# Kernel optimization log

Hardware: AMD Instinct MI355X
Metric: run time of the kernel (lower is better)

Reference implementation:

```python
import jax, jax.numpy as jnp
import numpy as np

B, T, D1, D2, DM, V, K = 2, 512, 256, 128, 1024, 32000, 4
SCALE = 0.05  # keep tanh/sigmoid out of full saturation with randn params


def setup_inputs() -> dict:
    key = jax.random.key(0)
    ks = jax.random.split(key, 7)
    s = lambda k, shape: SCALE * jax.random.normal(k, shape, dtype=jnp.float32)
    return {
        "gc": jax.random.normal(ks[0], (B, T, D1), dtype=jnp.float32),
        "H": s(ks[1], (K, DM, D1)),
        "U": s(ks[2], (K, D2, D1)),
        "v": s(ks[3], (V, D2)),
        "u": s(ks[4], (K, D1)),
        "b": s(ks[5], (V, K)),
        "emb": s(ks[6], (V, DM)),
    }


def reference(gc, H, U, v, u, b, emb):
    # gc: (B,T,D1)
    hc = jnp.tanh(jnp.einsum('kdi,bti->btkd', H, gc))        # (B,T,K,DM)
    tU = jnp.tanh(jnp.einsum('kji,bti->btkj', U, gc))        # (B,T,K,D2)
    # token- and context-dependent gate logits: (B,T,V,K)
    lc = (jnp.einsum('vj,btkj->btvk', v, tU)
          + jnp.einsum('ki,bti->btk', u, gc)[:, :, None, :]
          + b[None, None])
    gamma = jax.nn.sigmoid(lc[..., :K - 1])                  # (B,T,V,3)
    g0, g1, g2 = gamma[..., 0], gamma[..., 1], gamma[..., 2]
    # sigmoid-tree mixture priors: (B,T,V,K)
    pi = jnp.stack([g0 * g1, g0 * (1.0 - g1),
                    (1.0 - g0) * g2, (1.0 - g0) * (1.0 - g2)], axis=-1)
    # contract hc with embeddings per gate FIRST (avoids btikj blow-up),
    # then weight by pi -- same math as the original pi (x) emb outer product.
    dots = jnp.einsum('btkd,vd->btvk', hc, emb)              # (B,T,V,K)
    logits = jnp.sum(pi * dots, axis=-1)                     # (B,T,V)
    return jax.nn.softmax(logits, axis=-1)
```

## Files before the change

kernel.cpp:

```cpp
#include <hip/hip_runtime.h>
#include <math.h>

namespace {

typedef _Float16 f16;
typedef _Float16 f16x8 __attribute__((ext_vector_type(8)));
typedef float    f32x4 __attribute__((ext_vector_type(4)));

constexpr int kBT = 1024, kD1 = 256, kD2 = 128, kDM = 1024, kV = 32000, kK = 4;
constexpr int AR = kBT * kK;
constexpr int ROWS_H = kK * kDM;
constexpr int ROWS_U = kK * kD2;
constexpr int ROWS_ALL = ROWS_H + ROWS_U + kK;
constexpr int SLICES = 8;
constexpr int SLICE_ROWS = (ROWS_ALL + SLICES - 1) / SLICES;
constexpr int NBY = kV / 128;

__global__ __launch_bounds__(256) void prep_gemm(
    const float* __restrict__ gc, const float* __restrict__ Hm,
    const float* __restrict__ Um, const float* __restrict__ um,
    f16* __restrict__ hc, f16* __restrict__ tu, float* __restrict__ ug)
{
    __shared__ float sgc[8][kD1];
    const int btBase = blockIdx.x * 8;
    for (int idx = threadIdx.x; idx < 8 * kD1; idx += 256)
        sgc[idx / kD1][idx % kD1] = gc[(size_t)btBase * kD1 + idx];
    __syncthreads();

    const int rStart = blockIdx.y * SLICE_ROWS;
    int rEnd = rStart + SLICE_ROWS;
    if (rEnd > ROWS_ALL) rEnd = ROWS_ALL;
    for (int r = rStart + (int)threadIdx.x; r < rEnd; r += 256) {
        const float* wrow;
        if (r < ROWS_H)               wrow = Hm + (size_t)r * kD1;
        else if (r < ROWS_H + ROWS_U) wrow = Um + (size_t)(r - ROWS_H) * kD1;
        else                          wrow = um + (size_t)(r - ROWS_H - ROWS_U) * kD1;

        float acc[8] = {0.f,0.f,0.f,0.f,0.f,0.f,0.f,0.f};
        for (int i = 0; i < kD1; i += 4) {
            const float4 w = *reinterpret_cast<const float4*>(wrow + i);
            #pragma unroll
            for (int b = 0; b < 8; ++b) {
                const float4 g = *reinterpret_cast<const float4*>(&sgc[b][i]);
                acc[b] = fmaf(w.x, g.x, acc[b]);
                acc[b] = fmaf(w.y, g.y, acc[b]);
                acc[b] = fmaf(w.z, g.z, acc[b]);
                acc[b] = fmaf(w.w, g.w, acc[b]);
            }
        }
        #pragma unroll
        for (int b = 0; b < 8; ++b) {
            const int bt = btBase + b;
            if (r < ROWS_H) {
                const int k = r >> 10, d = r & 1023;
                hc[((size_t)(bt * kK + k) << 10) + d] = (f16)tanhf(acc[b]);
            } else if (r < ROWS_H + ROWS_U) {
                const int r2 = r - ROWS_H;
                const int k = r2 >> 7, j = r2 & 127;
                tu[(size_t)(bt * kK + k) * kD2 + j] = (f16)tanhf(acc[b]);
            } else {
                ug[bt * kK + (r - ROWS_H - ROWS_U)] = acc[b];
            }
        }
    }
}

__global__ __launch_bounds__(256) void cvt_kernel(
    const float* __restrict__ src, f16* __restrict__ dst, int n8)
{
    const int i = blockIdx.x * 256 + threadIdx.x;
    if (i >= n8) return;
    const float4 x0 = *reinterpret_cast<const float4*>(src + (size_t)i * 8);
    const float4 x1 = *reinterpret_cast<const float4*>(src + (size_t)i * 8 + 4);
    union { f16 h[8]; uint4 v; } u;
    u.h[0] = (f16)x0.x; u.h[1] = (f16)x0.y; u.h[2] = (f16)x0.z; u.h[3] = (f16)x0.w;
    u.h[4] = (f16)x1.x; u.h[5] = (f16)x1.y; u.h[6] = (f16)x1.z; u.h[7] = (f16)x1.w;
    *reinterpret_cast<uint4*>(dst + (size_t)i * 8) = u.v;
}

__device__ __forceinline__ uint packf16x2(float a, float b) {
    union { f16 h[2]; uint u; } z;
    z.h[0] = (f16)a; z.h[1] = (f16)b;
    return z.u;
}

__global__ __launch_bounds__(256, 2) void fused_mfma(
    const f16* __restrict__ hc,  const f16* __restrict__ tu,
    const f16* __restrict__ v16, const f16* __restrict__ e16,
    const float* __restrict__ ug, const float* __restrict__ bmat,
    f16* __restrict__ lg16, float* __restrict__ psum)
{
    __shared__ __align__(16) f16 sA[2][128 * 64];
    __shared__ __align__(16) f16 sB[2][128 * 64];

    const int tid  = threadIdx.x;
    const int lane = tid & 63;
    const int wave = tid >> 6;
    const int fr = lane & 15, fq = lane >> 4;
    const int wrow = wave >> 1, wcol = wave & 1;
    const int aRowBase = blockIdx.x * 128;
    const int vBase    = blockIdx.y * 128;
    const int btB      = blockIdx.x * 32 + wrow * 16;

    const int srow = lane >> 3;
    const int scol = ((lane & 7) ^ srow) * 8;

    const f16* gApt = tu  + (size_t)(aRowBase + wave * 32 + srow) * kD2 + scol;
    const f16* gBpt = v16 + (size_t)(vBase    + wave * 32 + srow) * kD2 + scol;
    const f16* sApt = hc  + (size_t)(aRowBase + wave * 32 + srow) * kDM + scol;
    const f16* sBpt = e16 + (size_t)(vBase    + wave * 32 + srow) * kDM + scol;

    f16* dA = &sA[0][0] + wave * 4 * 512;
    f16* dB = &sB[0][0] + wave * 4 * 512;

#define GLD(SRC, DST)                                                         \
    __builtin_amdgcn_global_load_lds(                                         \
        (const __attribute__((address_space(1))) void*)(SRC),                 \
        (__attribute__((address_space(3))) void*)(DST), 16, 0, 0)

    auto stage_gate = [&](int t) {
        #pragma unroll
        for (int i = 0; i < 4; ++i) {
            GLD(gApt + t * 64 + i * 8 * kD2, dA + t * 8192 + i * 512);
            GLD(gBpt + t * 64 + i * 8 * kD2, dB + t * 8192 + i * 512);
        }
    };
    auto stage_dots = [&](int buf) {
        #pragma unroll
        for (int i = 0; i < 4; ++i) {
            GLD(sApt + i * 8 * kDM, dA + buf * 8192 + i * 512);
            GLD(sBpt + i * 8 * kDM, dB + buf * 8192 + i * 512);
        }
        sApt += 64; sBpt += 64;
    };

    const int ps0 = (fq ^ (fr & 7)) * 8;
    const int ps1 = ((4 + fq) ^ (fr & 7)) * 8;
    const f16* rA0 = &sA[0][0] + (wrow * 64 + fr) * 64 + ps0;
    const f16* rA1 = &sA[0][0] + (wrow * 64 + fr) * 64 + ps1;
    const f16* rB0 = &sB[0][0] + (wcol * 64 + fr) * 64 + ps0;
    const f16* rB1 = &sB[0][0] + (wcol * 64 + fr) * 64 + ps1;

    auto mmStep = [&](f32x4 (&acc)[4][4], int q) {
        const int qo = q * 8192;
        {
            f16x8 a[4], b[4];
            #pragma unroll
            for (int m = 0; m < 4; ++m)
                a[m] = *reinterpret_cast<const f16x8*>(rA0 + qo + m * 1024);
            #pragma unroll
            for (int n = 0; n < 4; ++n)
                b[n] = *reinterpret_cast<const f16x8*>(rB0 + qo + n * 1024);
            __builtin_amdgcn_s_setprio(1);
            #pragma unroll
            for (int m = 0; m < 4; ++m)
                #pragma unroll
                for (int n = 0; n < 4; ++n)
                    acc[m][n] = __builtin_amdgcn_mfma_f32_16x16x32_f16(
                        a[m], b[n], acc[m][n], 0, 0, 0);
            __builtin_amdgcn_s_setprio(0);
        }
        {
            f16x8 a[4], b[4];
            #pragma unroll
            for (int m = 0; m < 4; ++m)
                a[m] = *reinterpret_cast<const f16x8*>(rA1 + qo + m * 1024);
            #pragma unroll
            for (int n = 0; n < 4; ++n)
                b[n] = *reinterpret_cast<const f16x8*>(rB1 + qo + n * 1024);
            __builtin_amdgcn_s_setprio(1);
            #pragma unroll
            for (int m = 0; m < 4; ++m)
                #pragma unroll
                for (int n = 0; n < 4; ++n)
                    acc[m][n] = __builtin_amdgcn_mfma_f32_16x16x32_f16(
                        a[m], b[n], acc[m][n], 0, 0, 0);
            __builtin_amdgcn_s_setprio(0);
        }
    };

#define WAITBAR(VM)                                                           \
    asm volatile("s_waitcnt vmcnt(" VM ")" ::: "memory");                     \
    __builtin_amdgcn_s_barrier();                                             \
    asm volatile("" ::: "memory");
#define ENDBAR                                                                \
    asm volatile("" ::: "memory");                                            \
    __builtin_amdgcn_s_barrier();                                             \
    asm volatile("" ::: "memory");

    const f32x4 zz = {0.f, 0.f, 0.f, 0.f};

    f32x4 gacc[4][4];
    #pragma unroll
    for (int m = 0; m < 4; ++m)
        #pragma unroll
        for (int n = 0; n < 4; ++n) gacc[m][n] = zz;

    stage_gate(0);
    stage_gate(1);          WAITBAR("8")  mmStep(gacc, 0);  ENDBAR
    stage_dots(0);          WAITBAR("8")  mmStep(gacc, 1);  ENDBAR

    uint pi01[4][4], pi23[4][4];
    {
        float4 bb[4];
        #pragma unroll
        for (int n = 0; n < 4; ++n)
            bb[n] = *reinterpret_cast<const float4*>(
                bmat + (size_t)(vBase + wcol * 64 + n * 16 + fr) * 4);
        #pragma unroll
        for (int m = 0; m < 4; ++m) {
            const float4 ugv = *reinterpret_cast<const float4*>(
                ug + (btB + m * 4 + fq) * 4);
            #pragma unroll
            for (int n = 0; n < 4; ++n) {
                const float l0 = gacc[m][n][0] + ugv.x + bb[n].x;
                const float l1 = gacc[m][n][1] + ugv.y + bb[n].y;
                const float l2 = gacc[m][n][2] + ugv.z + bb[n].z;
                const float g0 = 1.f / (1.f + __expf(-l0));
                const float g1 = 1.f / (1.f + __expf(-l1));
                const float g2 = 1.f / (1.f + __expf(-l2));
                pi01[m][n] = packf16x2(g0 * g1, g0 * (1.f - g1));
                pi23[m][n] = packf16x2((1.f - g0) * g2, (1.f - g0) * (1.f - g2));
            }
        }
    }

    f32x4 dacc[4][4];
    #pragma unroll
    for (int m = 0; m < 4; ++m)
        #pragma unroll
        for (int n = 0; n < 4; ++n) dacc[m][n] = zz;

    for (int it = 0; it < 7; ++it) {
        stage_dots(1);      WAITBAR("8")  mmStep(dacc, 0);  ENDBAR
        stage_dots(0);      WAITBAR("8")  mmStep(dacc, 1);  ENDBAR
    }
    stage_dots(1);          WAITBAR("8")  mmStep(dacc, 0);  ENDBAR
                            WAITBAR("0")  mmStep(dacc, 1);
#undef WAITBAR
#undef ENDBAR
#undef GLD

    #pragma unroll
    for (int m = 0; m < 4; ++m) {
        const int bt = btB + m * 4 + fq;
        float es = 0.f;
        #pragma unroll
        for (int n = 0; n < 4; ++n) {
            const int v = vBase + wcol * 64 + n * 16 + fr;
            union { uint u; f16 h[2]; } p01, p23;
            p01.u = pi01[m][n]; p23.u = pi23[m][n];
            const float lg = (float)p01.h[0] * dacc[m][n][0]
                           + (float)p01.h[1] * dacc[m][n][1]
                           + (float)p23.h[0] * dacc[m][n][2]
                           + (float)p23.h[1] * dacc[m][n][3];
            const f16 lh = (f16)lg;
            lg16[(size_t)bt * kV + v] = lh;
            es += __expf((float)lh);
        }
        es += __shfl_xor(es, 1);
        es += __shfl_xor(es, 2);
        es += __shfl_xor(es, 4);
        es += __shfl_xor(es, 8);
        if (fr == 0)
            psum[(size_t)bt * 512 + blockIdx.y * 2 + wcol] = es;
    }
}

__global__ __launch_bounds__(256) void softmax_kernel(
    float* __restrict__ out, const f16* __restrict__ lg16,
    const float* __restrict__ psum)
{
    __shared__ float red[4];
    const int bt = blockIdx.x;
    const f16* row16 = lg16 + (size_t)bt * kV;
    float* row = out + (size_t)bt * kV;
    const int tid = threadIdx.x;

    float s = 0.f;
    for (int i = tid; i < 2 * NBY; i += 256) s += psum[(size_t)bt * 512 + i];
    #pragma unroll
    for (int o = 1; o < 64; o <<= 1) s += __shfl_xor(s, o);
    if ((tid & 63) == 0) red[tid >> 6] = s;
    __syncthreads();
    s = red[0] + red[1] + red[2] + red[3];
    const float inv = 1.f / s;

    for (int i = tid * 8; i < kV; i += 2048) {
        union { uint4 v; f16 h[8]; } u;
        u.v = *reinterpret_cast<const uint4*>(row16 + i);
        float4 y0, y1;
        y0.x = __expf((float)u.h[0]) * inv;
        y0.y = __expf((float)u.h[1]) * inv;
        y0.z = __expf((float)u.h[2]) * inv;
        y0.w = __expf((float)u.h[3]) * inv;
        y1.x = __expf((float)u.h[4]) * inv;
        y1.y = __expf((float)u.h[5]) * inv;
        y1.z = __expf((float)u.h[6]) * inv;
        y1.w = __expf((float)u.h[7]) * inv;
        *reinterpret_cast<float4*>(row + i)     = y0;
        *reinterpret_cast<float4*>(row + i + 4) = y1;
    }
}

}

extern "C" void kernel_launch(void* const* d_in, const int* in_sizes, int n_in,
                              void* d_out, int out_size, void* d_ws, size_t ws_size,
                              hipStream_t stream)
{
    (void)in_sizes; (void)n_in; (void)out_size; (void)ws_size;
    const float* gc   = (const float*)d_in[0];
    const float* Hm   = (const float*)d_in[1];
    const float* Um   = (const float*)d_in[2];
    const float* vmat = (const float*)d_in[3];
    const float* um   = (const float*)d_in[4];
    const float* bmat = (const float*)d_in[5];
    const float* emb  = (const float*)d_in[6];
    float* out = (float*)d_out;

    size_t off = 0;
    auto take = [&](size_t bytes) -> char* {
        char* p = (char*)d_ws + off;
        off += (bytes + 255) & ~(size_t)255;
        return p;
    };
    f16*   hc   = (f16*)  take((size_t)AR * kDM * 2);
    f16*   tu   = (f16*)  take((size_t)AR * kD2 * 2);
    f16*   v16  = (f16*)  take((size_t)kV * kD2 * 2);
    f16*   e16  = (f16*)  take((size_t)kV * kDM * 2);
    float* ug   = (float*)take((size_t)AR * 4);
    float* psum = (float*)take((size_t)kBT * 512 * 4);
    f16*   lg16 = (f16*)  take((size_t)kBT * kV * 2);

    prep_gemm<<<dim3(kBT / 8, SLICES), 256, 0, stream>>>(gc, Hm, Um, um, hc, tu, ug);
    cvt_kernel<<<(kV * kD2 / 8 + 255) / 256, 256, 0, stream>>>(vmat, v16, kV * kD2 / 8);
    cvt_kernel<<<(kV * kDM / 8 + 255) / 256, 256, 0, stream>>>(emb, e16, kV * kDM / 8);
    fused_mfma<<<dim3(AR / 128, NBY), 256, 0, stream>>>(
        hc, tu, v16, e16, ug, bmat, lg16, psum);
    softmax_kernel<<<dim3(kBT), 256, 0, stream>>>(out, lg16, psum);
}
```

Before: 533.7 us.

## Halve MFMA K-tile to 32 and merge prep and convert kernels

The main GEMM kernel's LDS K-tile shrinks from 64 to 32 halves per stage. That halves shared memory per block and drops the 2-blocks-per-SM launch bound, aiming for higher occupancy. The swizzle, load mapping and pipeline (twice as many stages, with a different vmcnt wait) are reworked to match. The three preprocessing launches (projection GEMM plus two fp32-to-fp16 conversions) are merged into one kernel to save launch overhead and let them run concurrently. The cost is more barriers per unit of work and less MFMA work between each synchronisation.

```diff
diff --git a/kernel.cpp b/kernel.cpp
--- a/kernel.cpp
+++ b/kernel.cpp
@@ -16,18 +16,48 @@
 constexpr int SLICE_ROWS = (ROWS_ALL + SLICES - 1) / SLICES;
 constexpr int NBY = kV / 128;
 
-__global__ __launch_bounds__(256) void prep_gemm(
+constexpr int PREP_BLOCKS = (kBT / 8) * SLICES;
+constexpr int CVTV_BLOCKS = (kV * kD2 / 8) / 256;
+constexpr int CVTE_BLOCKS = (kV * kDM / 8) / 256;
+
+__global__ __launch_bounds__(256) void prep_cvt(
     const float* __restrict__ gc, const float* __restrict__ Hm,
     const float* __restrict__ Um, const float* __restrict__ um,
-    f16* __restrict__ hc, f16* __restrict__ tu, float* __restrict__ ug)
+    const float* __restrict__ vmat, const float* __restrict__ emb,
+    f16* __restrict__ hc, f16* __restrict__ tu, float* __restrict__ ug,
+    f16* __restrict__ v16, f16* __restrict__ e16)
 {
     __shared__ float sgc[8][kD1];
-    const int btBase = blockIdx.x * 8;
+    const int bid = blockIdx.x;
+
+    if (bid >= PREP_BLOCKS) {
+        const float* src;
+        f16* dst;
+        int i;
+        if (bid < PREP_BLOCKS + CVTV_BLOCKS) {
+            src = vmat; dst = v16;
+            i = (bid - PREP_BLOCKS) * 256 + threadIdx.x;
+        } else {
+            src = emb; dst = e16;
+            i = (bid - PREP_BLOCKS - CVTV_BLOCKS) * 256 + threadIdx.x;
+        }
+        const float4 x0 = *reinterpret_cast<const float4*>(src + (size_t)i * 8);
+        const float4 x1 = *reinterpret_cast<const float4*>(src + (size_t)i * 8 + 4);
+        union { f16 h[8]; uint4 v; } u;
+        u.h[0] = (f16)x0.x; u.h[1] = (f16)x0.y; u.h[2] = (f16)x0.z; u.h[3] = (f16)x0.w;
+        u.h[4] = (f16)x1.x; u.h[5] = (f16)x1.y; u.h[6] = (f16)x1.z; u.h[7] = (f16)x1.w;
+        *reinterpret_cast<uint4*>(dst + (size_t)i * 8) = u.v;
+        return;
+    }
+
+    const int pbx = bid & 127;
+    const int pby = bid >> 7;
+    const int btBase = pbx * 8;
     for (int idx = threadIdx.x; idx < 8 * kD1; idx += 256)
         sgc[idx / kD1][idx % kD1] = gc[(size_t)btBase * kD1 + idx];
     __syncthreads();
 
-    const int rStart = blockIdx.y * SLICE_ROWS;
+    const int rStart = pby * SLICE_ROWS;
     int rEnd = rStart + SLICE_ROWS;
     if (rEnd > ROWS_ALL) rEnd = ROWS_ALL;
     for (int r = rStart + (int)threadIdx.x; r < rEnd; r += 256) {
@@ -65,33 +95,20 @@
     }
 }
 
-__global__ __launch_bounds__(256) void cvt_kernel(
-    const float* __restrict__ src, f16* __restrict__ dst, int n8)
-{
-    const int i = blockIdx.x * 256 + threadIdx.x;
-    if (i >= n8) return;
-    const float4 x0 = *reinterpret_cast<const float4*>(src + (size_t)i * 8);
-    const float4 x1 = *reinterpret_cast<const float4*>(src + (size_t)i * 8 + 4);
-    union { f16 h[8]; uint4 v; } u;
-    u.h[0] = (f16)x0.x; u.h[1] = (f16)x0.y; u.h[2] = (f16)x0.z; u.h[3] = (f16)x0.w;
-    u.h[4] = (f16)x1.x; u.h[5] = (f16)x1.y; u.h[6] = (f16)x1.z; u.h[7] = (f16)x1.w;
-    *reinterpret_cast<uint4*>(dst + (size_t)i * 8) = u.v;
-}
-
 __device__ __forceinline__ uint packf16x2(float a, float b) {
     union { f16 h[2]; uint u; } z;
     z.h[0] = (f16)a; z.h[1] = (f16)b;
     return z.u;
 }
 
-__global__ __launch_bounds__(256, 2) void fused_mfma(
+__global__ __launch_bounds__(256) void fused_mfma(
     const f16* __restrict__ hc,  const f16* __restrict__ tu,
     const f16* __restrict__ v16, const f16* __restrict__ e16,
     const float* __restrict__ ug, const float* __restrict__ bmat,
     f16* __restrict__ lg16, float* __restrict__ psum)
 {
-    __shared__ __align__(16) f16 sA[2][128 * 64];
-    __shared__ __align__(16) f16 sB[2][128 * 64];
+    __shared__ __align__(16) f16 sA[2][128 * 32];
+    __shared__ __align__(16) f16 sB[2][128 * 32];
 
     const int tid  = threadIdx.x;
     const int lane = tid & 63;
@@ -102,16 +119,16 @@
     const int vBase    = blockIdx.y * 128;
     const int btB      = blockIdx.x * 32 + wrow * 16;
 
-    const int srow = lane >> 3;
-    const int scol = ((lane & 7) ^ srow) * 8;
+    const int srow = lane >> 2;
+    const int scol = ((lane & 3) ^ ((lane >> 3) & 3)) * 8;
 
     const f16* gApt = tu  + (size_t)(aRowBase + wave * 32 + srow) * kD2 + scol;
     const f16* gBpt = v16 + (size_t)(vBase    + wave * 32 + srow) * kD2 + scol;
     const f16* sApt = hc  + (size_t)(aRowBase + wave * 32 + srow) * kDM + scol;
     const f16* sBpt = e16 + (size_t)(vBase    + wave * 32 + srow) * kDM + scol;
 
-    f16* dA = &sA[0][0] + wave * 4 * 512;
-    f16* dB = &sB[0][0] + wave * 4 * 512;
+    f16* dA = &sA[0][0] + wave * 2 * 512;
+    f16* dB = &sB[0][0] + wave * 2 * 512;
 
 #define GLD(SRC, DST)                                                         \
     __builtin_amdgcn_global_load_lds(                                         \
@@ -120,67 +137,44 @@
 
     auto stage_gate = [&](int t) {
         #pragma unroll
-        for (int i = 0; i < 4; ++i) {
-            GLD(gApt + t * 64 + i * 8 * kD2, dA + t * 8192 + i * 512);
-            GLD(gBpt + t * 64 + i * 8 * kD2, dB + t * 8192 + i * 512);
+        for (int i = 0; i < 2; ++i) {
+            GLD(gApt + t * 32 + i * 16 * kD2, dA + (t & 1) * 4096 + i * 512);
+            GLD(gBpt + t * 32 + i * 16 * kD2, dB + (t & 1) * 4096 + i * 512);
         }
     };
     auto stage_dots = [&](int buf) {
         #pragma unroll
-        for (int i = 0; i < 4; ++i) {
-            GLD(sApt + i * 8 * kDM, dA + buf * 8192 + i * 512);
-            GLD(sBpt + i * 8 * kDM, dB + buf * 8192 + i * 512);
-        }
-        sApt += 64; sBpt += 64;
+        for (int i = 0; i < 2; ++i) {
+            GLD(sApt + i * 16 * kDM, dA + buf * 4096 + i * 512);
+            GLD(sBpt + i * 16 * kDM, dB + buf * 4096 + i * 512);
+        }
+        sApt += 32; sBpt += 32;
     };
 
-    const int ps0 = (fq ^ (fr & 7)) * 8;
-    const int ps1 = ((4 + fq) ^ (fr & 7)) * 8;
-    const f16* rA0 = &sA[0][0] + (wrow * 64 + fr) * 64 + ps0;
-    const f16* rA1 = &sA[0][0] + (wrow * 64 + fr) * 64 + ps1;
-    const f16* rB0 = &sB[0][0] + (wcol * 64 + fr) * 64 + ps0;
-    const f16* rB1 = &sB[0][0] + (wcol * 64 + fr) * 64 + ps1;
+    const int ps = (fq ^ ((fr >> 1) & 3)) * 8;
+    const f16* rA = &sA[0][0] + (wrow * 64 + fr) * 32 + ps;
+    const f16* rB = &sB[0][0] + (wcol * 64 + fr) * 32 + ps;
 
     auto mmStep = [&](f32x4 (&acc)[4][4], int q) {
-        const int qo = q * 8192;
-        {
-            f16x8 a[4], b[4];
-            #pragma unroll
-            for (int m = 0; m < 4; ++m)
-                a[m] = *reinterpret_cast<const f16x8*>(rA0 + qo + m * 1024);
+        const int qo = q * 4096;
+        f16x8 b[4];
+        #pragma unroll
+        for (int n = 0; n < 4; ++n)
+            b[n] = *reinterpret_cast<const f16x8*>(rB + qo + n * 512);
+        __builtin_amdgcn_s_setprio(1);
+        #pragma unroll
+        for (int m = 0; m < 4; ++m) {
+            const f16x8 a = *reinterpret_cast<const f16x8*>(rA + qo + m * 512);
             #pragma unroll
             for (int n = 0; n < 4; ++n)
-                b[n] = *reinterpret_cast<const f16x8*>(rB0 + qo + n * 1024);
-            __builtin_amdgcn_s_setprio(1);
-            #pragma unroll
-            for (int m = 0; m < 4; ++m)
-                #pragma unroll
-                for (int n = 0; n < 4; ++n)
-                    acc[m][n] = __builtin_amdgcn_mfma_f32_16x16x32_f16(
-                        a[m], b[n], acc[m][n], 0, 0, 0);
-            __builtin_amdgcn_s_setprio(0);
-        }
-        {
-            f16x8 a[4], b[4];
-            #pragma unroll
-            for (int m = 0; m < 4; ++m)
-                a[m] = *reinterpret_cast<const f16x8*>(rA1 + qo + m * 1024);
-            #pragma unroll
-            for (int n = 0; n < 4; ++n)
-                b[n] = *reinterpret_cast<const f16x8*>(rB1 + qo + n * 1024);
-            __builtin_amdgcn_s_setprio(1);
-            #pragma unroll
-            for (int m = 0; m < 4; ++m)
-                #pragma unroll
-                for (int n = 0; n < 4; ++n)
-                    acc[m][n] = __builtin_amdgcn_mfma_f32_16x16x32_f16(
-                        a[m], b[n], acc[m][n], 0, 0, 0);
-            __builtin_amdgcn_s_setprio(0);
-        }
+                acc[m][n] = __builtin_amdgcn_mfma_f32_16x16x32_f16(
+                    a, b[n], acc[m][n], 0, 0, 0);
+        }
+        __builtin_amdgcn_s_setprio(0);
     };
 
-#define WAITBAR(VM)                                                           \
-    asm volatile("s_waitcnt vmcnt(" VM ")" ::: "memory");                     \
+#define WAITBAR                                                               \
+    asm volatile("s_waitcnt vmcnt(4)" ::: "memory");                          \
     __builtin_amdgcn_s_barrier();                                             \
     asm volatile("" ::: "memory");
 #define ENDBAR                                                                \
@@ -197,8 +191,10 @@
         for (int n = 0; n < 4; ++n) gacc[m][n] = zz;
 
     stage_gate(0);
-    stage_gate(1);          WAITBAR("8")  mmStep(gacc, 0);  ENDBAR
-    stage_dots(0);          WAITBAR("8")  mmStep(gacc, 1);  ENDBAR
+    stage_gate(1);      WAITBAR  mmStep(gacc, 0);  ENDBAR
+    stage_gate(2);      WAITBAR  mmStep(gacc, 1);  ENDBAR
+    stage_gate(3);      WAITBAR  mmStep(gacc, 0);  ENDBAR
+    stage_dots(0);      WAITBAR  mmStep(gacc, 1);  ENDBAR
 
     uint pi01[4][4], pi23[4][4];
     {
@@ -231,12 +227,15 @@
         #pragma unroll
         for (int n = 0; n < 4; ++n) dacc[m][n] = zz;
 
-    for (int it = 0; it < 7; ++it) {
-        stage_dots(1);      WAITBAR("8")  mmStep(dacc, 0);  ENDBAR
-        stage_dots(0);      WAITBAR("8")  mmStep(dacc, 1);  ENDBAR
-    }
-    stage_dots(1);          WAITBAR("8")  mmStep(dacc, 0);  ENDBAR
-                            WAITBAR("0")  mmStep(dacc, 1);
+    for (int it = 0; it < 15; ++it) {
+        stage_dots(1);  WAITBAR  mmStep(dacc, 0);  ENDBAR
+        stage_dots(0);  WAITBAR  mmStep(dacc, 1);  ENDBAR
+    }
+    stage_dots(1);      WAITBAR  mmStep(dacc, 0);  ENDBAR
+    asm volatile("s_waitcnt vmcnt(0)" ::: "memory");
+    __builtin_amdgcn_s_barrier();
+    asm volatile("" ::: "memory");
+    mmStep(dacc, 1);
 #undef WAITBAR
 #undef ENDBAR
 #undef GLD
@@ -333,9 +332,8 @@
     float* psum = (float*)take((size_t)kBT * 512 * 4);
     f16*   lg16 = (f16*)  take((size_t)kBT * kV * 2);
 
-    prep_gemm<<<dim3(kBT / 8, SLICES), 256, 0, stream>>>(gc, Hm, Um, um, hc, tu, ug);
-    cvt_kernel<<<(kV * kD2 / 8 + 255) / 256, 256, 0, stream>>>(vmat, v16, kV * kD2 / 8);
-    cvt_kernel<<<(kV * kDM / 8 + 255) / 256, 256, 0, stream>>>(emb, e16, kV * kDM / 8);
+    prep_cvt<<<dim3(PREP_BLOCKS + CVTV_BLOCKS + CVTE_BLOCKS), 256, 0, stream>>>(
+        gc, Hm, Um, um, vmat, emb, hc, tu, ug, v16, e16);
     fused_mfma<<<dim3(AR / 128, NBY), 256, 0, stream>>>(
         hc, tu, v16, e16, ug, bmat, lg16, psum);
     softmax_kernel<<<dim3(kBT), 256, 0, stream>>>(out, lg16, psum);
```

After: 609.1 us. 14.1% more time.
